# Kernel tuning notes

Hardware: AMD Instinct MI355X
Metric: run time of the kernel (lower is better)

Reference implementation:

```python
import jax, jax.numpy as jnp
import numpy as np

H = 64          # hiddens_dims
K = 3           # Chebyshev order
B = 16          # graphs in batch
NPG = 16384     # nodes per graph
N = B * NPG     # total nodes
E = 2_097_152   # total edges
R = 2191        # num_residues (hard-coded in source)
E_REF = R * 16
HALF = N // 2   # backbone count == sidechain count (mask is balanced per graph)


def _lin(k, fan_in, shape):
    return jax.random.uniform(k, shape, jnp.float32, -1.0, 1.0) / np.sqrt(fan_in)


def setup_inputs() -> dict:
    key = jax.random.key(0)
    ks = jax.random.split(key, 40)
    inp = {}
    inp["x"] = jax.random.normal(ks[0], (N, 3), jnp.float32)
    inp["edge_index"] = jax.random.randint(ks[1], (2, E), 0, N)
    inp["batch"] = jnp.repeat(jnp.arange(B, dtype=jnp.int32), NPG)
    blk = jnp.concatenate([jnp.ones((NPG // 2,), bool), jnp.zeros((NPG // 2,), bool)])
    inp["mask"] = jnp.tile(blk, B)  # backbone=True first half of each graph block
    inp["x_ref"] = jax.random.normal(ks[2], (R, 3), jnp.float32)
    inp["edgeref"] = jax.random.randint(ks[3], (2, E_REF), 0, R)
    i = 4
    for name, cin in [("cw0", 3), ("cw1", H), ("cw2", H), ("rw0", 3), ("rw1", H), ("rw2", H)]:
        inp[name] = _lin(ks[i], cin, (K, cin, H)); i += 1
        inp[name.replace("w", "b")] = jnp.zeros((H,), jnp.float32)  # ChebConv bias init = zeros
    for name, cin, cout in [("mlp_w", 2 * H, H), ("mlpP2_w", 2 * H, H),
                            ("rep0_w", H, H), ("rep1_w", H, H), ("rep2_w", H, 3)]:
        inp[name] = _lin(ks[i], cin, (cin, cout)); i += 1
        inp[name.replace("_w", "_b")] = _lin(ks[i], cin, (cout,)); i += 1
    return inp


def cheb_conv(x, edge_index, W, b, n):
    # PyG ChebConv with sym normalization, lambda_max=2: L_hat = -D^-1/2 A D^-1/2 (diag = 0)
    row, col = edge_index[0], edge_index[1]
    deg = jax.ops.segment_sum(jnp.ones_like(x[:, 0])[row] * 0 + 1.0, row, num_segments=n)
    dinv = jnp.where(deg > 0, jax.lax.rsqrt(jnp.maximum(deg, 1e-12)), 0.0)
    w = -(dinv[row] * dinv[col])  # [E]

    def prop(h):  # L_hat @ h via gather + segment_sum
        return jax.ops.segment_sum(w[:, None] * h[col], row, num_segments=n)

    Tx0 = x
    out = Tx0 @ W[0]
    Tx1 = prop(x)
    out = out + Tx1 @ W[1]
    for k in range(2, K):
        Tx2 = 2.0 * prop(Tx1) - Tx0
        out = out + Tx2 @ W[k]
        Tx0, Tx1 = Tx1, Tx2
    return out + b


def _forward(x, edge_index, mask, x_ref, edgeref,
             cw0, cb0, cw1, cb1, cw2, cb2, rw0, rb0, rw1, rb1, rw2, rb2,
             mlp_w, mlp_b, mlpP2_w, mlpP2_b,
             rep0_w, rep0_b, rep1_w, rep1_b, rep2_w, rep2_b):
    # main GNN stack (tanh after all but last; dropout is identity in eval)
    h = jnp.tanh(cheb_conv(x, edge_index, cw0, cb0, N))
    h = jnp.tanh(cheb_conv(h, edge_index, cw1, cb1, N))
    h = cheb_conv(h, edge_index, cw2, cb2, N)

    bb_idx = jnp.nonzero(mask, size=HALF)[0]
    sc_idx = jnp.nonzero(~mask, size=HALF)[0]
    x_bb = h[bb_idx].reshape(B, -1, H).mean(axis=1)[:, None, :]  # [B,1,H]
    x_sc = h[sc_idx].reshape(B, -1, H).mean(axis=1)[:, None, :]  # [B,1,H]

    # reference-graph stack: source bug makes `conv2 != self.convs[-1]` always True,
    # so tanh follows every convRef layer
    r = jnp.tanh(cheb_conv(x_ref, edgeref, rw0, rb0, R))
    r = jnp.tanh(cheb_conv(r, edgeref, rw1, rb1, R))
    r = jnp.tanh(cheb_conv(r, edgeref, rw2, rb2, R))
    r = jnp.broadcast_to(r[None], (B, R, H))

    bb_rep = jnp.broadcast_to(x_bb, (B, R, H))
    phase1 = jnp.concatenate([r, bb_rep], axis=-1) @ mlp_w + mlp_b        # [B,R,H]
    sc_rep = jnp.broadcast_to(x_sc, (B, R, H))
    phase2 = jnp.concatenate([phase1, sc_rep], axis=-1) @ mlpP2_w + mlpP2_b  # [B,R,H]

    res = phase2.reshape(-1, H)
    res = jax.nn.relu(res @ rep0_w + rep0_b)
    res = jax.nn.relu(res @ rep1_w + rep1_b)
    res = jax.nn.relu(res @ rep2_w + rep2_b)  # [B*R, 3]
    return res.reshape(-1, 3), x_bb, x_sc


def reference(x, edge_index, batch, mask, x_ref, edgeref,
              cw0, cb0, cw1, cb1, cw2, cb2, rw0, rb0, rw1, rb1, rw2, rb2,
              mlp_w, mlp_b, mlpP2_w, mlpP2_b,
              rep0_w, rep0_b, rep1_w, rep1_b, rep2_w, rep2_b):
    del batch  # only used for len(batch.unique()) == B, a static constant here
    return _forward(x, edge_index, mask, x_ref, edgeref,
                    cw0, cb0, cw1, cb1, cw2, cb2, rw0, rb0, rw1, rb1, rw2, rb2,
                    mlp_w, mlp_b, mlpP2_w, mlpP2_b,
                    rep0_w, rep0_b, rep1_w, rep1_b, rep2_w, rep2_b)
```

## Files before the change

kernel.cpp:

```cpp
#include <hip/hip_runtime.h>
#include <hip/hip_fp16.h>
#include <math.h>

#define NN 262144
#define NE 2097152
#define RR 2191
#define ER (RR*16)
#define NB 16
#define BRR (NB*RR)
#define OUT_RES (BRR*3)

typedef __attribute__((ext_vector_type(8))) _Float16 half8;
typedef __attribute__((ext_vector_type(4))) float f32x4;

__global__ void k_histprep(const int* __restrict__ eM, int* __restrict__ degM,
                           unsigned char* __restrict__ rankM,
                           const int* __restrict__ eR, int* __restrict__ degR,
                           unsigned char* __restrict__ rankR,
                           const float* __restrict__ cw1, const float* __restrict__ cw2,
                           const float* __restrict__ rw1, const float* __restrict__ rw2,
                           float* __restrict__ weffC2, float* __restrict__ weffR1,
                           float* __restrict__ weffR2, _Float16* __restrict__ wfragC1,
                           const float* __restrict__ x, float4* __restrict__ x4,
                           const float* __restrict__ x_ref, float4* __restrict__ xr4){
  int b = blockIdx.x, t = threadIdx.x;
  if (b < 2048){
    for (int i = b*256 + t; i < NE; i += 2048*256){
      int old = atomicAdd(&degM[eM[i]], 1);
      rankM[i] = (unsigned char)old;
    }
  } else if (b < 2112){
    for (int i = (b-2048)*256 + t; i < ER; i += 64*256){
      int old = atomicAdd(&degR[eR[i]], 1);
      rankR[i] = (unsigned char)old;
    }
  } else if (b < 2160){
    int y = (b - 2112) >> 4;
    int i = ((b - 2112) & 15)*256 + t;
    const float* W = (y == 0) ? cw2 : (y == 1) ? rw1 : rw2;
    float* D       = (y == 0) ? weffC2 : (y == 1) ? weffR1 : weffR2;
    D[i]        = W[i] - W[8192 + i];
    D[4096 + i] = W[4096 + i];
    D[8192 + i] = 2.0f * W[8192 + i];
  } else if (b < 2208){
    int i = (b - 2160)*256 + t;
    int reg = i & 7, lane = (i >> 3) & 63, nt = (i >> 9) & 3, kc = i >> 11;
    int m = kc >> 1;
    int kin = (kc & 1)*32 + ((lane >> 4) & 3)*8 + reg;
    int n = nt*16 + (lane & 15);
    float eff;
    if      (m == 0) eff = cw1[kin*64 + n] - cw1[8192 + kin*64 + n];
    else if (m == 1) eff = cw1[4096 + kin*64 + n];
    else             eff = 2.0f * cw1[8192 + kin*64 + n];
    wfragC1[i] = (_Float16)eff;
  } else if (b < 3232){
    int i = (b - 2208)*256 + t;
    if (i < NN) x4[i] = make_float4(x[i*3], x[i*3+1], x[i*3+2], 0.0f);
  } else {
    int i = (b - 3232)*256 + t;
    if (i < RR) xr4[i] = make_float4(x_ref[i*3], x_ref[i*3+1], x_ref[i*3+2], 0.0f);
  }
}

__global__ void k_scan1(const int* __restrict__ deg, int* __restrict__ rowptr,
                        int* __restrict__ partials, float* __restrict__ dinv){
  __shared__ int s[256];
  int t = threadIdx.x; int i = blockIdx.x*256 + t;
  int v = deg[i]; s[t] = v; __syncthreads();
  dinv[i] = v > 0 ? 1.0f/sqrtf((float)v) : 0.0f;
  for (int off = 1; off < 256; off <<= 1){
    int x = (t >= off) ? s[t-off] : 0; __syncthreads();
    s[t] += x; __syncthreads();
  }
  rowptr[i] = s[t] - v;
  if (t == 255) partials[blockIdx.x] = s[255];
}

__global__ void __launch_bounds__(1024) k_scan2m(int* __restrict__ partials,
                                                 const int* __restrict__ degR,
                                                 int* __restrict__ rowptrR,
                                                 float* __restrict__ dinvR){
  __shared__ int s[1024];
  int t = threadIdx.x;
  if (blockIdx.x == 0){
    int v = partials[t]; s[t] = v; __syncthreads();
    for (int off = 1; off < 1024; off <<= 1){
      int x = (t >= off) ? s[t-off] : 0; __syncthreads();
      s[t] += x; __syncthreads();
    }
    partials[t] = s[t] - v;
  } else {
    int carry = 0;
    for (int base = 0; base < RR; base += 1024){
      int idx = base + t;
      int v = (idx < RR) ? degR[idx] : 0;
      if (idx < RR) dinvR[idx] = v > 0 ? 1.0f/sqrtf((float)v) : 0.0f;
      s[t] = v; __syncthreads();
      for (int off = 1; off < 1024; off <<= 1){
        int x = (t >= off) ? s[t-off] : 0; __syncthreads();
        s[t] += x; __syncthreads();
      }
      if (idx < RR) rowptrR[idx] = carry + s[t] - v;
      carry += s[1023];
      __syncthreads();
    }
    if (t == 0) rowptrR[RR] = carry;
  }
}

__global__ void k_scan3(int* __restrict__ rowptr, const int* __restrict__ partials){
  int t = threadIdx.x; int i = blockIdx.x*256 + t;
  rowptr[i] += partials[blockIdx.x];
  if (i == 0) rowptr[NN] = NE;
}

__global__ void k_scatter2(const int* __restrict__ eM, const float* __restrict__ dinv,
                           const int* __restrict__ rowptr, const unsigned char* __restrict__ rankM,
                           int2* __restrict__ pair,
                           const int* __restrict__ eR, const float* __restrict__ dinvR,
                           const int* __restrict__ rowptrR, const unsigned char* __restrict__ rankR,
                           int2* __restrict__ pairR){
  int b = blockIdx.x;
  if (b < 2048){
    for (int i = b*256 + threadIdx.x; i < NE; i += 2048*256){
      int r = eM[i], c = eM[NE + i];
      int pos = rowptr[r] + rankM[i];
      unsigned wbits = (unsigned)__float_as_int(-dinv[r]*dinv[c]);
      long long v = (unsigned)c | ((long long)wbits << 32);
      __builtin_nontemporal_store(v, (long long*)(pair + pos));
    }
  } else {
    for (int i = (b-2048)*256 + threadIdx.x; i < ER; i += 64*256){
      int r = eR[i], c = eR[ER + i];
      int pos = rowptrR[r] + rankR[i];
      unsigned wbits = (unsigned)__float_as_int(-dinvR[r]*dinvR[c]);
      long long v = (unsigned)c | ((long long)wbits << 32);
      __builtin_nontemporal_store(v, (long long*)(pairR + pos));
    }
  }
}

__device__ __forceinline__ void prop3_body(const float4* __restrict__ h, float4* __restrict__ y,
                                           const int* __restrict__ rowptr,
                                           const int2* __restrict__ pair, int i){
  float a0 = 0.f, a1 = 0.f, a2 = 0.f;
  int s = rowptr[i], e = rowptr[i+1];
  int p = s;
  for (; p + 4 <= e; p += 4){
    int2 q0 = pair[p], q1 = pair[p+1], q2 = pair[p+2], q3 = pair[p+3];
    float4 v0 = h[q0.x], v1 = h[q1.x], v2 = h[q2.x], v3 = h[q3.x];
    float w0 = __int_as_float(q0.y), w1 = __int_as_float(q1.y);
    float w2 = __int_as_float(q2.y), w3 = __int_as_float(q3.y);
    a0 = fmaf(w0,v0.x, fmaf(w1,v1.x, fmaf(w2,v2.x, fmaf(w3,v3.x, a0))));
    a1 = fmaf(w0,v0.y, fmaf(w1,v1.y, fmaf(w2,v2.y, fmaf(w3,v3.y, a1))));
    a2 = fmaf(w0,v0.z, fmaf(w1,v1.z, fmaf(w2,v2.z, fmaf(w3,v3.z, a2))));
  }
  for (; p < e; p++){
    int2 q = pair[p]; float wv = __int_as_float(q.y);
    float4 v = h[q.x];
    a0 = fmaf(wv, v.x, a0); a1 = fmaf(wv, v.y, a1); a2 = fmaf(wv, v.z, a2);
  }
  y[i] = make_float4(a0, a1, a2, 0.0f);
}

__device__ __forceinline__ void combine3_body(const float4* __restrict__ x,
                                              const float4* __restrict__ t1,
                                              const float4* __restrict__ t2,
                                              const float* __restrict__ W,
                                              const float* __restrict__ bias,
                                              int i, int lane, float* accout){
  float4 px = x[i], p1 = t1[i], p2 = t2[i];
  const float* fx = (const float*)&px;
  const float* f1 = (const float*)&p1;
  const float* f2 = (const float*)&p2;
  float acc = bias[lane];
  #pragma unroll
  for (int j = 0; j < 3; j++){
    float x0 = fx[j], x1 = f1[j];
    float x2 = 2.0f*f2[j] - x0;
    acc += x0*W[      j*64 + lane]
         + x1*W[192 + j*64 + lane]
         + x2*W[384 + j*64 + lane];
  }
  *accout = tanhf(acc);
}

__device__ __forceinline__ void prop64f_body(const float* __restrict__ h, float* __restrict__ y,
                                             const int* __restrict__ rowptr,
                                             const int2* __restrict__ pair, int i, int lane){
  float acc = 0.f;
  int s = rowptr[i], e = rowptr[i+1];
  int p = s;
  for (; p + 4 <= e; p += 4){
    int2 q0 = pair[p], q1 = pair[p+1], q2 = pair[p+2], q3 = pair[p+3];
    float v0 = h[(size_t)q0.x*64 + lane], v1 = h[(size_t)q1.x*64 + lane];
    float v2 = h[(size_t)q2.x*64 + lane], v3 = h[(size_t)q3.x*64 + lane];
    acc = fmaf(__int_as_float(q0.y),v0, fmaf(__int_as_float(q1.y),v1,
          fmaf(__int_as_float(q2.y),v2, fmaf(__int_as_float(q3.y),v3, acc))));
  }
  for (; p < e; p++){
    int2 q = pair[p];
    acc = fmaf(__int_as_float(q.y), h[(size_t)q.x*64 + lane], acc);
  }
  y[(size_t)i*64 + lane] = acc;
}

__device__ __forceinline__ void combine64f_body(const float* __restrict__ A,
                                                const float* __restrict__ Bm,
                                                const float* __restrict__ C,
                                                const float* __restrict__ Weff,
                                                const float* __restrict__ bias,
                                                float* __restrict__ out, int n,
                                                int blk, int t){
  int lane = t & 63;
  int wid  = __builtin_amdgcn_readfirstlane(t >> 6);
  int half_ = wid & 1;
  int row  = blk*128 + (wid >> 1)*64 + lane;
  bool active = (row < n);
  float acc[32];
  #pragma unroll
  for (int c = 0; c < 32; c++) acc[c] = bias[half_*32 + c];
  if (active){
    #pragma unroll 1
    for (int m = 0; m < 3; m++){
      const float* src = (m == 0 ? A : (m == 1 ? Bm : C)) + (size_t)row*64;
      const float* Wm  = Weff + m*4096 + half_*32;
      #pragma unroll 1
      for (int k4 = 0; k4 < 16; k4++){
        float4 a4 = *(const float4*)(src + k4*4);
        const float* wk = Wm + k4*256;
        #pragma unroll
        for (int kk = 0; kk < 4; kk++){
          float a = (kk == 0) ? a4.x : (kk == 1) ? a4.y : (kk == 2) ? a4.z : a4.w;
          #pragma unroll
          for (int c = 0; c < 32; c++)
            acc[c] = fmaf(a, wk[kk*64 + c], acc[c]);
        }
      }
    }
  }
  __syncthreads();
  if (active){
    float* o = out + (size_t)row*64 + half_*32;
    #pragma unroll
    for (int c = 0; c < 32; c++) o[c] = tanhf(acc[c]);
  }
}

__global__ void k_prop3m(const float4* __restrict__ hM, float4* __restrict__ yM,
                         const int* __restrict__ rowptr, const int2* __restrict__ pair,
                         const float4* __restrict__ hR, float4* __restrict__ yR,
                         const int* __restrict__ rowptrR, const int2* __restrict__ pairR){
  int b = blockIdx.x, t = threadIdx.x;
  if (b < 1024){
    prop3_body(hM, yM, rowptr, pair, b*256 + t);
  } else {
    int i = (b - 1024)*256 + t;
    if (i < RR) prop3_body(hR, yR, rowptrR, pairR, i);
  }
}

__global__ void k_combine3m(const float4* __restrict__ x, const float4* __restrict__ t1,
                            const float4* __restrict__ t2, const float* __restrict__ cW,
                            const float* __restrict__ cb, __half* __restrict__ outM,
                            const float4* __restrict__ xr, const float4* __restrict__ r1,
                            const float4* __restrict__ r2, const float* __restrict__ rW,
                            const float* __restrict__ rb, float* __restrict__ outR){
  int b = blockIdx.x, t = threadIdx.x, lane = t & 63;
  if (b < 65536){
    int i = b*4 + (t >> 6);
    float v; combine3_body(x, t1, t2, cW, cb, i, lane, &v);
    outM[(size_t)i*64 + lane] = __float2half_rn(v);
  } else {
    int i = (b - 65536)*4 + (t >> 6);
    if (i < RR){
      float v; combine3_body(xr, r1, r2, rW, rb, i, lane, &v);
      outR[(size_t)i*64 + lane] = v;
    }
  }
}

__global__ void __launch_bounds__(256) k_prop64m(
    const uint4* __restrict__ h4, uint4* __restrict__ y4,
    const int* __restrict__ rowptr, const int2* __restrict__ pair,
    const float* __restrict__ hR, float* __restrict__ yR,
    const int* __restrict__ rowptrR, const int2* __restrict__ pairR){
  int b = blockIdx.x, t = threadIdx.x;
  if (b >= 8192){
    int i = (b - 8192)*4 + (t >> 6);
    if (i < RR) prop64f_body(hR, yR, rowptrR, pairR, i, t & 63);
    return;
  }
  int sub = t & 7;
  int row = b*32 + (t >> 3);
  int s = rowptr[row], e = rowptr[row+1];
  float ac[8];
  #pragma unroll
  for (int k = 0; k < 8; k++) ac[k] = 0.f;
  int p = s;
  for (; p + 8 <= e; p += 8){
    int2 q[8]; uint4 v[8];
    #pragma unroll
    for (int j = 0; j < 8; j++) q[j] = pair[p+j];
    #pragma unroll
    for (int j = 0; j < 8; j++) v[j] = h4[(size_t)q[j].x*8 + sub];
    #pragma unroll
    for (int j = 0; j < 8; j++){
      float wv = __int_as_float(q[j].y);
      #pragma unroll
      for (int k = 0; k < 4; k++){
        float2 f = __half22float2(((const __half2*)&v[j])[k]);
        ac[2*k]   = fmaf(wv, f.x, ac[2*k]);
        ac[2*k+1] = fmaf(wv, f.y, ac[2*k+1]);
      }
    }
  }
  for (; p + 4 <= e; p += 4){
    int2 q[4]; uint4 v[4];
    #pragma unroll
    for (int j = 0; j < 4; j++) q[j] = pair[p+j];
    #pragma unroll
    for (int j = 0; j < 4; j++) v[j] = h4[(size_t)q[j].x*8 + sub];
    #pragma unroll
    for (int j = 0; j < 4; j++){
      float wv = __int_as_float(q[j].y);
      #pragma unroll
      for (int k = 0; k < 4; k++){
        float2 f = __half22float2(((const __half2*)&v[j])[k]);
        ac[2*k]   = fmaf(wv, f.x, ac[2*k]);
        ac[2*k+1] = fmaf(wv, f.y, ac[2*k+1]);
      }
    }
  }
  for (; p < e; p++){
    int2 q = pair[p];
    float wv = __int_as_float(q.y);
    uint4 v = h4[(size_t)q.x*8 + sub];
    #pragma unroll
    for (int k = 0; k < 4; k++){
      float2 f = __half22float2(((const __half2*)&v)[k]);
      ac[2*k]   = fmaf(wv, f.x, ac[2*k]);
      ac[2*k+1] = fmaf(wv, f.y, ac[2*k+1]);
    }
  }
  uint4 r;
  #pragma unroll
  for (int k = 0; k < 4; k++){
    __half2 hp = __floats2half2_rn(ac[2*k], ac[2*k+1]);
    ((unsigned*)&r)[k] = *(unsigned*)&hp;
  }
  y4[(size_t)row*8 + sub] = r;
}

__global__ void __launch_bounds__(256) k_combine64mm(
    const __half* A, const __half* B, const __half* C,
    const _Float16* __restrict__ wfrag, const float* __restrict__ bias,
    __half* out, int ntiles, int wavestride,
    const float* __restrict__ rA, const float* __restrict__ rB, const float* __restrict__ rC,
    const float* __restrict__ weffR, const float* __restrict__ biasR,
    float* __restrict__ outR){
  int t = threadIdx.x;
  if (blockIdx.x >= 1024){
    combine64f_body(rA, rB, rC, weffR, biasR, outR, RR, blockIdx.x - 1024, t);
    return;
  }
  int lane = t & 63;
  int wv = blockIdx.x*4 + (t >> 6);
  half8 bf[24];
  #pragma unroll
  for (int i = 0; i < 24; i++)
    bf[i] = *(const half8*)(wfrag + ((size_t)(i*64 + lane))*8);
  int col = lane & 15, grp = (lane >> 4) & 3;
  float b0 = bias[col], b1 = bias[16+col], b2 = bias[32+col], b3 = bias[48+col];
  for (int tile = wv; tile < ntiles; tile += wavestride){
    size_t rb = (size_t)tile*16;
    f32x4 acc0 = {b0,b0,b0,b0}, acc1 = {b1,b1,b1,b1};
    f32x4 acc2 = {b2,b2,b2,b2}, acc3 = {b3,b3,b3,b3};
    #pragma unroll
    for (int kc = 0; kc < 6; kc++){
      const __half* s = (kc < 2) ? A : (kc < 4) ? B : C;
      half8 a = *(const half8*)(s + (rb + col)*64 + (kc & 1)*32 + grp*8);
      acc0 = __builtin_amdgcn_mfma_f32_16x16x32_f16(a, bf[kc*4+0], acc0, 0,0,0);
      acc1 = __builtin_amdgcn_mfma_f32_16x16x32_f16(a, bf[kc*4+1], acc1, 0,0,0);
      acc2 = __builtin_amdgcn_mfma_f32_16x16x32_f16(a, bf[kc*4+2], acc2, 0,0,0);
      acc3 = __builtin_amdgcn_mfma_f32_16x16x32_f16(a, bf[kc*4+3], acc3, 0,0,0);
    }
    __half* o = out + (rb + grp*4)*64;
    #pragma unroll
    for (int r = 0; r < 4; r++){
      o[(size_t)r*64 +      col] = __float2half_rn(tanhf(acc0[r]));
      o[(size_t)r*64 + 16 + col] = __float2half_rn(tanhf(acc1[r]));
      o[(size_t)r*64 + 32 + col] = __float2half_rn(tanhf(acc2[r]));
      o[(size_t)r*64 + 48 + col] = __float2half_rn(tanhf(acc3[r]));
    }
  }
}

__global__ void k_tail3(const __half2* __restrict__ hA, const __half2* __restrict__ hB,
                        const __half2* __restrict__ hC, float* __restrict__ pA,
                        float* __restrict__ pB, float* __restrict__ pC,
                        const float* __restrict__ rA, const float* __restrict__ rB,
                        const float* __restrict__ rC, const float* __restrict__ weffR,
                        const float* __restrict__ biasR, float* __restrict__ outR){
  int b = blockIdx.x, t = threadIdx.x;
  if (b >= 1536){
    combine64f_body(rA, rB, rC, weffR, biasR, outR, RR, b - 1536, t);
    return;
  }
  int y = b >> 9;
  const __half2* src = (y == 0) ? hA : (y == 1) ? hB : hC;
  float* dst         = (y == 0) ? pA : (y == 1) ? pB : pC;
  int blk = b & 511;
  int chunk = blk & 15, seg = blk >> 4;
  int ch2 = t & 31, rsub = t >> 5;
  int base = seg*8192 + chunk*512;
  float ax = 0.f, ay = 0.f;
  for (int j = 0; j < 64; j++){
    int row = base + rsub + j*8;
    float2 v = __half22float2(src[(size_t)row*32 + ch2]);
    ax += v.x; ay += v.y;
  }
  __shared__ float sx[256], sy[256];
  sx[t] = ax; sy[t] = ay; __syncthreads();
  if (t < 32){
    float tx = 0.f, ty = 0.f;
    #pragma unroll
    for (int j = 0; j < 8; j++){ tx += sx[ch2 + j*32]; ty += sy[ch2 + j*32]; }
    int bb = seg >> 1, half_ = seg & 1;
    atomicAdd(&dst[half_*1024 + bb*64 + ch2*2],     tx);
    atomicAdd(&dst[half_*1024 + bb*64 + ch2*2 + 1], ty);
  }
}

__global__ void k_cpr(const float* __restrict__ pA, const float* __restrict__ pB,
                      const float* __restrict__ pC, const float* __restrict__ weff,
                      const float* __restrict__ bias, float* __restrict__ xbbsc,
                      float* __restrict__ dout,
                      const float* __restrict__ refA, const float* __restrict__ mlp_w,
                      const float* __restrict__ mlp2_w, const float* __restrict__ rep0_w,
                      float* __restrict__ rt3a){
  int b = blockIdx.x, t = threadIdx.x;
  if (b < 8){
    int i = b*256 + t;
    int pr = i >> 6, c = i & 63;
    const float* a = pA + pr*64;
    const float* bb = pB + pr*64;
    const float* cc = pC + pr*64;
    float v = 0.f;
    for (int k = 0; k < 64; k++){
      v = fmaf(a[k],  weff[        k*64 + c], v);
      v = fmaf(bb[k], weff[4096 +  k*64 + c], v);
      v = fmaf(cc[k], weff[8192 +  k*64 + c], v);
    }
    v = v*(1.0f/8192.0f) + bias[c];
    xbbsc[i] = v;
    dout[OUT_RES + i] = v;
  } else {
    int lane = t & 63;
    int i = (b - 8)*4 + (t >> 6);
    if (i >= RR) return;
    float v = refA[i*64 + lane];
    float a = 0.f;
    #pragma unroll
    for (int k = 0; k < 64; k++) a += __shfl(v, k, 64) * mlp_w[k*64 + lane];
    float bb = 0.f;
    #pragma unroll
    for (int k = 0; k < 64; k++) bb += __shfl(a, k, 64) * mlp2_w[k*64 + lane];
    float c = 0.f;
    #pragma unroll
    for (int k = 0; k < 64; k++) c += __shfl(bb, k, 64) * rep0_w[k*64 + lane];
    rt3a[i*64 + lane] = c;
  }
}

__global__ void k_bbchain(const float* __restrict__ xbbsc,
                          const float* __restrict__ mlp_w,  const float* __restrict__ mlp_b,
                          const float* __restrict__ mlp2_w, const float* __restrict__ mlp2_b,
                          const float* __restrict__ rep0_w, const float* __restrict__ rep0_b,
                          float* __restrict__ bt3a){
  int t = threadIdx.x, lane = t & 63;
  int i = blockIdx.x*4 + (t >> 6);
  if (i >= NB) return;
  float vbb = xbbsc[i*64 + lane];
  float vsc = xbbsc[1024 + i*64 + lane];
  float a = mlp_b[lane];
  #pragma unroll
  for (int k = 0; k < 64; k++) a += __shfl(vbb, k, 64) * mlp_w[4096 + k*64 + lane];
  float b = mlp2_b[lane];
  #pragma unroll
  for (int k = 0; k < 64; k++) b += __shfl(a, k, 64) * mlp2_w[k*64 + lane];
  #pragma unroll
  for (int k = 0; k < 64; k++) b += __shfl(vsc, k, 64) * mlp2_w[4096 + k*64 + lane];
  float c = rep0_b[lane];
  #pragma unroll
  for (int k = 0; k < 64; k++) c += __shfl(b, k, 64) * rep0_w[k*64 + lane];
  bt3a[i*64 + lane] = c;
}

__global__ void k_final(const float* __restrict__ rt3, const float* __restrict__ bt3,
                        const float* __restrict__ W1, const float* __restrict__ b1,
                        const float* __restrict__ W2, const float* __restrict__ b2,
                        float* __restrict__ dout){
  int t = threadIdx.x, lane = t & 63;
  int g = blockIdx.x*4 + (t >> 6);
  if (g >= BRR) return;
  int b = g / RR, r = g - b*RR;
  float m = rt3[r*64 + lane] + bt3[b*64 + lane];
  m = fmaxf(m, 0.0f);
  float acc = b1[lane];
  #pragma unroll
  for (int k = 0; k < 64; k++) acc += __shfl(m, k, 64) * W1[k*64 + lane];
  float u = fmaxf(acc, 0.0f);
  float p0 = u*W2[lane*3+0], p1 = u*W2[lane*3+1], p2 = u*W2[lane*3+2];
  #pragma unroll
  for (int off = 32; off > 0; off >>= 1){
    p0 += __shfl_xor(p0, off, 64);
    p1 += __shfl_xor(p1, off, 64);
    p2 += __shfl_xor(p2, off, 64);
  }
  if (lane == 0){
    dout[g*3+0] = fmaxf(p0 + b2[0], 0.0f);
    dout[g*3+1] = fmaxf(p1 + b2[1], 0.0f);
    dout[g*3+2] = fmaxf(p2 + b2[2], 0.0f);
  }
}

extern "C" void kernel_launch(void* const* d_in, const int* in_sizes, int n_in,
                              void* d_out, int out_size, void* d_ws, size_t ws_size,
                              hipStream_t stream){
  const float* x     = (const float*)d_in[0];
  const int*   eidx  = (const int*)d_in[1];
  const float* x_ref = (const float*)d_in[4];
  const int*   eref  = (const int*)d_in[5];
  const float* cw0 = (const float*)d_in[6],  *cb0 = (const float*)d_in[7];
  const float* cw1 = (const float*)d_in[8],  *cb1 = (const float*)d_in[9];
  const float* cw2 = (const float*)d_in[10], *cb2 = (const float*)d_in[11];
  const float* rw0 = (const float*)d_in[12], *rb0 = (const float*)d_in[13];
  const float* rw1 = (const float*)d_in[14], *rb1 = (const float*)d_in[15];
  const float* rw2 = (const float*)d_in[16], *rb2 = (const float*)d_in[17];
  const float* mlp_w  = (const float*)d_in[18], *mlp_b  = (const float*)d_in[19];
  const float* mlp2_w = (const float*)d_in[20], *mlp2_b = (const float*)d_in[21];
  const float* rep0_w = (const float*)d_in[22], *rep0_b = (const float*)d_in[23];
  const float* rep1_w = (const float*)d_in[24], *rep1_b = (const float*)d_in[25];
  const float* rep2_w = (const float*)d_in[26], *rep2_b = (const float*)d_in[27];
  float* out = (float*)d_out;

  char* w = (char*)d_ws;
  size_t off = 0;
  auto alloc = [&](size_t bytes)->void*{
    void* p = w + off;
    off = (off + bytes + 255) & ~(size_t)255;
    return p;
  };
  int*   deg     = (int*)  alloc(NN*4);
  int*   degR    = (int*)  alloc(RR*4);
  float* poolA   = (float*)alloc(2048*4);
  float* poolB   = (float*)alloc(2048*4);
  float* poolC   = (float*)alloc(2048*4);
  size_t zero_bytes = off;

  int*   rowptr   = (int*)  alloc((NN+1)*4);
  int*   partials = (int*)  alloc(1024*4);
  int*   rowptrR  = (int*)  alloc((RR+1)*4);
  float* dinv     = (float*)alloc(NN*4);
  float* dinvR    = (float*)alloc(RR*4);
  unsigned char* rankM = (unsigned char*)alloc(NE);
  unsigned char* rankR = (unsigned char*)alloc(ER);
  int2*  cpair    = (int2*) alloc((size_t)NE*8);
  int2*  cpairR   = (int2*) alloc((size_t)ER*8);
  float4* x4      = (float4*)alloc((size_t)NN*16);
  float4* t1_4    = (float4*)alloc((size_t)NN*16);
  float4* t2_4    = (float4*)alloc((size_t)NN*16);
  float4* xr4     = (float4*)alloc((size_t)RR*16);
  float4* rt1_4   = (float4*)alloc((size_t)RR*16);
  float4* rt2_4   = (float4*)alloc((size_t)RR*16);
  __half* hA      = (__half*)alloc((size_t)NN*64*2);
  __half* hB      = (__half*)alloc((size_t)NN*64*2);
  __half* hC      = (__half*)alloc((size_t)NN*64*2);
  float* refA     = (float*)alloc(RR*64*4);
  float* refB     = (float*)alloc(RR*64*4);
  float* refC     = (float*)alloc(RR*64*4);
  float* xbbsc    = (float*)alloc(2048*4);
  float* rt3a     = (float*)alloc(RR*64*4);
  float* bt3a     = (float*)alloc(NB*64*4);
  float* weffC2   = (float*)alloc(12288*4);
  float* weffR1   = (float*)alloc(12288*4);
  float* weffR2   = (float*)alloc(12288*4);
  _Float16* wfragC1 = (_Float16*)alloc(12288*2);
  (void)ws_size; (void)in_sizes; (void)n_in; (void)out_size;

  hipMemsetAsync(d_ws, 0, zero_bytes, stream);

  k_histprep<<<3241, 256, 0, stream>>>(eidx, deg, rankM, eref, degR, rankR,
                                       cw1, cw2, rw1, rw2,
                                       weffC2, weffR1, weffR2, wfragC1,
                                       x, x4, x_ref, xr4);
  k_scan1<<<1024, 256, 0, stream>>>(deg, rowptr, partials, dinv);
  k_scan2m<<<2, 1024, 0, stream>>>(partials, degR, rowptrR, dinvR);
  k_scan3<<<1024, 256, 0, stream>>>(rowptr, partials);
  k_scatter2<<<2112, 256, 0, stream>>>(eidx, dinv, rowptr, rankM, cpair,
                                       eref, dinvR, rowptrR, rankR, cpairR);

  k_prop3m<<<1033, 256, 0, stream>>>(x4, t1_4, rowptr, cpair, xr4, rt1_4, rowptrR, cpairR);
  k_prop3m<<<1033, 256, 0, stream>>>(t1_4, t2_4, rowptr, cpair, rt1_4, rt2_4, rowptrR, cpairR);
  k_combine3m<<<66084, 256, 0, stream>>>(x4, t1_4, t2_4, cw0, cb0, hA,
                                         xr4, rt1_4, rt2_4, rw0, rb0, refA);
  k_prop64m<<<8740, 256, 0, stream>>>((const uint4*)hA, (uint4*)hB, rowptr, cpair,
                                      refA, refB, rowptrR, cpairR);
  k_prop64m<<<8740, 256, 0, stream>>>((const uint4*)hB, (uint4*)hC, rowptr, cpair,
                                      refB, refC, rowptrR, cpairR);
  k_combine64mm<<<1042, 256, 0, stream>>>(hA, hB, hC, wfragC1, cb1, hA, NN/16, 4096,
                                          refA, refB, refC, weffR1, rb1, refA);
  k_prop64m<<<8740, 256, 0, stream>>>((const uint4*)hA, (uint4*)hB, rowptr, cpair,
                                      refA, refB, rowptrR, cpairR);
  k_prop64m<<<8740, 256, 0, stream>>>((const uint4*)hB, (uint4*)hC, rowptr, cpair,
                                      refB, refC, rowptrR, cpairR);
  k_tail3<<<1554, 256, 0, stream>>>((const __half2*)hA, (const __half2*)hB, (const __half2*)hC,
                                    poolA, poolB, poolC,
                                    refA, refB, refC, weffR2, rb2, refA);
  k_cpr<<<556, 256, 0, stream>>>(poolA, poolB, poolC, weffC2, cb2, xbbsc, out,
                                 refA, mlp_w, mlp2_w, rep0_w, rt3a);
  k_bbchain<<<4, 256, 0, stream>>>(xbbsc, mlp_w, mlp_b, mlp2_w, mlp2_b, rep0_w, rep0_b, bt3a);
  k_final<<<(BRR+3)/4, 256, 0, stream>>>(rt3a, bt3a, rep1_w, rep1_b, rep2_w, rep2_b, out);
}
```

Before: 673.1 us.

## Replace final Chebyshev propagation with pooled column-weight sums and nontemporal edge loads

The last graph propagation (hC = L·hB) is only ever consumed through per-graph, per-half pooling, so it is replaced algebraically. A per-source sigma table (sum of edge weights into each of 32 graph-half segments) is accumulated with atomics inside the first propagation launch, and pooled L·hB is then computed as sigma-weighted sums of hB. This removes one full 64-wide gather-propagation pass. The CSR pair loads become nontemporal, and the small tail kernels are merged into fewer launches. The cost is a 32 MB sigma buffer that must be zeroed each call, plus 2M float atomics, and more work in the reduction blocks.

```diff
diff --git a/kernel.cpp b/kernel.cpp
--- a/kernel.cpp
+++ b/kernel.cpp
@@ -12,6 +12,12 @@
 
 typedef __attribute__((ext_vector_type(8))) _Float16 half8;
 typedef __attribute__((ext_vector_type(4))) float f32x4;
+
+__device__ __forceinline__ int2 ntp(const int2* p){
+  long long v = __builtin_nontemporal_load((const long long*)p);
+  int2 r; r.x = (int)(unsigned)(v & 0xffffffffll); r.y = (int)(unsigned)((unsigned long long)v >> 32);
+  return r;
+}
 
 __global__ void k_histprep(const int* __restrict__ eM, int* __restrict__ degM,
                            unsigned char* __restrict__ rankM,
@@ -147,7 +153,7 @@
   int s = rowptr[i], e = rowptr[i+1];
   int p = s;
   for (; p + 4 <= e; p += 4){
-    int2 q0 = pair[p], q1 = pair[p+1], q2 = pair[p+2], q3 = pair[p+3];
+    int2 q0 = ntp(pair+p), q1 = ntp(pair+p+1), q2 = ntp(pair+p+2), q3 = ntp(pair+p+3);
     float4 v0 = h[q0.x], v1 = h[q1.x], v2 = h[q2.x], v3 = h[q3.x];
     float w0 = __int_as_float(q0.y), w1 = __int_as_float(q1.y);
     float w2 = __int_as_float(q2.y), w3 = __int_as_float(q3.y);
@@ -284,8 +290,18 @@
     const uint4* __restrict__ h4, uint4* __restrict__ y4,
     const int* __restrict__ rowptr, const int2* __restrict__ pair,
     const float* __restrict__ hR, float* __restrict__ yR,
-    const int* __restrict__ rowptrR, const int2* __restrict__ pairR){
+    const int* __restrict__ rowptrR, const int2* __restrict__ pairR,
+    const int* __restrict__ eidx, const float* __restrict__ dinv,
+    float* __restrict__ sigma){
   int b = blockIdx.x, t = threadIdx.x;
+  if (b >= 8740){
+    int sb = b - 8740;
+    for (int i = sb*256 + t; i < NE; i += 512*256){
+      int r = eidx[i], c = eidx[NE + i];
+      atomicAdd(&sigma[(size_t)c*32 + (r >> 13)], -dinv[r]*dinv[c]);
+    }
+    return;
+  }
   if (b >= 8192){
     int i = (b - 8192)*4 + (t >> 6);
     if (i < RR) prop64f_body(hR, yR, rowptrR, pairR, i, t & 63);
@@ -301,7 +317,7 @@
   for (; p + 8 <= e; p += 8){
     int2 q[8]; uint4 v[8];
     #pragma unroll
-    for (int j = 0; j < 8; j++) q[j] = pair[p+j];
+    for (int j = 0; j < 8; j++) q[j] = ntp(pair + p + j);
     #pragma unroll
     for (int j = 0; j < 8; j++) v[j] = h4[(size_t)q[j].x*8 + sub];
     #pragma unroll
@@ -318,7 +334,7 @@
   for (; p + 4 <= e; p += 4){
     int2 q[4]; uint4 v[4];
     #pragma unroll
-    for (int j = 0; j < 4; j++) q[j] = pair[p+j];
+    for (int j = 0; j < 4; j++) q[j] = ntp(pair + p + j);
     #pragma unroll
     for (int j = 0; j < 4; j++) v[j] = h4[(size_t)q[j].x*8 + sub];
     #pragma unroll
@@ -396,49 +412,86 @@
   }
 }
 
-__global__ void k_tail3(const __half2* __restrict__ hA, const __half2* __restrict__ hB,
-                        const __half2* __restrict__ hC, float* __restrict__ pA,
-                        float* __restrict__ pB, float* __restrict__ pC,
-                        const float* __restrict__ rA, const float* __restrict__ rB,
-                        const float* __restrict__ rC, const float* __restrict__ weffR,
-                        const float* __restrict__ biasR, float* __restrict__ outR){
+__global__ void __launch_bounds__(256) k_sigred(
+    const __half2* __restrict__ hA2, const __half2* __restrict__ hB2,
+    const __half* __restrict__ hBh, const float* __restrict__ sigma,
+    float* __restrict__ pA, float* __restrict__ pB, float* __restrict__ pC,
+    const float* __restrict__ rB, float* __restrict__ rC,
+    const int* __restrict__ rowptrR, const int2* __restrict__ pairR){
   int b = blockIdx.x, t = threadIdx.x;
-  if (b >= 1536){
-    combine64f_body(rA, rB, rC, weffR, biasR, outR, RR, b - 1536, t);
-    return;
-  }
-  int y = b >> 9;
-  const __half2* src = (y == 0) ? hA : (y == 1) ? hB : hC;
-  float* dst         = (y == 0) ? pA : (y == 1) ? pB : pC;
-  int blk = b & 511;
-  int chunk = blk & 15, seg = blk >> 4;
-  int ch2 = t & 31, rsub = t >> 5;
-  int base = seg*8192 + chunk*512;
-  float ax = 0.f, ay = 0.f;
-  for (int j = 0; j < 64; j++){
-    int row = base + rsub + j*8;
-    float2 v = __half22float2(src[(size_t)row*32 + ch2]);
-    ax += v.x; ay += v.y;
-  }
-  __shared__ float sx[256], sy[256];
-  sx[t] = ax; sy[t] = ay; __syncthreads();
-  if (t < 32){
-    float tx = 0.f, ty = 0.f;
-    #pragma unroll
-    for (int j = 0; j < 8; j++){ tx += sx[ch2 + j*32]; ty += sy[ch2 + j*32]; }
-    int bb = seg >> 1, half_ = seg & 1;
-    atomicAdd(&dst[half_*1024 + bb*64 + ch2*2],     tx);
-    atomicAdd(&dst[half_*1024 + bb*64 + ch2*2 + 1], ty);
-  }
-}
-
-__global__ void k_cpr(const float* __restrict__ pA, const float* __restrict__ pB,
-                      const float* __restrict__ pC, const float* __restrict__ weff,
-                      const float* __restrict__ bias, float* __restrict__ xbbsc,
-                      float* __restrict__ dout,
-                      const float* __restrict__ refA, const float* __restrict__ mlp_w,
-                      const float* __restrict__ mlp2_w, const float* __restrict__ rep0_w,
-                      float* __restrict__ rt3a){
+  if (b < 1024){
+    const __half2* src = (b < 512) ? hA2 : hB2;
+    float* dst = (b < 512) ? pA : pB;
+    int blk = b & 511;
+    int chunk = blk & 15, seg = blk >> 4;
+    int ch2 = t & 31, rsub = t >> 5;
+    int base = seg*8192 + chunk*512;
+    float ax = 0.f, ay = 0.f;
+    for (int j = 0; j < 64; j++){
+      int row = base + rsub + j*8;
+      float2 v = __half22float2(src[(size_t)row*32 + ch2]);
+      ax += v.x; ay += v.y;
+    }
+    __shared__ float sx[256], sy[256];
+    sx[t] = ax; sy[t] = ay; __syncthreads();
+    if (t < 32){
+      float tx = 0.f, ty = 0.f;
+      #pragma unroll
+      for (int j = 0; j < 8; j++){ tx += sx[ch2 + j*32]; ty += sy[ch2 + j*32]; }
+      int bb = seg >> 1, half_ = seg & 1;
+      atomicAdd(&dst[half_*1024 + bb*64 + ch2*2],     tx);
+      atomicAdd(&dst[half_*1024 + bb*64 + ch2*2 + 1], ty);
+    }
+  } else if (b < 1152){
+    int blk = b - 1024;
+    int ch = t & 63, jsub = t >> 6;
+    float acc[32];
+    #pragma unroll
+    for (int s = 0; s < 32; s++) acc[s] = 0.f;
+    int jend = blk*2048 + 2048;
+    for (int j = blk*2048 + jsub; j < jend; j += 4){
+      float bv = __half2float(hBh[(size_t)j*64 + ch]);
+      const float4* sg = (const float4*)(sigma + (size_t)j*32);
+      #pragma unroll
+      for (int sq = 0; sq < 8; sq++){
+        float4 s4 = sg[sq];
+        acc[sq*4+0] = fmaf(s4.x, bv, acc[sq*4+0]);
+        acc[sq*4+1] = fmaf(s4.y, bv, acc[sq*4+1]);
+        acc[sq*4+2] = fmaf(s4.z, bv, acc[sq*4+2]);
+        acc[sq*4+3] = fmaf(s4.w, bv, acc[sq*4+3]);
+      }
+    }
+    __shared__ float red[32][64];
+    if (jsub == 0){
+      #pragma unroll
+      for (int s = 0; s < 32; s++) red[s][ch] = acc[s];
+    }
+    __syncthreads();
+    #pragma unroll
+    for (int w = 1; w < 4; w++){
+      if (jsub == w){
+        #pragma unroll
+        for (int s = 0; s < 32; s++) red[s][ch] += acc[s];
+      }
+      __syncthreads();
+    }
+    for (int e = t; e < 2048; e += 256){
+      int s = e >> 6, c = e & 63;
+      atomicAdd(&pC[(s & 1)*1024 + (s >> 1)*64 + c], red[s][c]);
+    }
+  } else {
+    int i = (b - 1152)*4 + (t >> 6);
+    if (i < RR) prop64f_body(rB, rC, rowptrR, pairR, i, t & 63);
+  }
+}
+
+__global__ void k_cpr3(const float* __restrict__ pA, const float* __restrict__ pB,
+                       const float* __restrict__ pC, const float* __restrict__ weff,
+                       const float* __restrict__ bias, float* __restrict__ xbbsc,
+                       float* __restrict__ dout,
+                       const float* __restrict__ rA, const float* __restrict__ rB,
+                       const float* __restrict__ rC, const float* __restrict__ weffR,
+                       const float* __restrict__ biasR, float* __restrict__ outR){
   int b = blockIdx.x, t = threadIdx.x;
   if (b < 8){
     int i = b*256 + t;
@@ -456,8 +509,19 @@
     xbbsc[i] = v;
     dout[OUT_RES + i] = v;
   } else {
-    int lane = t & 63;
-    int i = (b - 8)*4 + (t >> 6);
+    combine64f_body(rA, rB, rC, weffR, biasR, outR, RR, b - 8, t);
+  }
+}
+
+__global__ void k_chains(const float* __restrict__ refA, const float* __restrict__ mlp_w,
+                         const float* __restrict__ mlp2_w, const float* __restrict__ rep0_w,
+                         float* __restrict__ rt3a,
+                         const float* __restrict__ xbbsc, const float* __restrict__ mlp_b,
+                         const float* __restrict__ mlp2_b, const float* __restrict__ rep0_b,
+                         float* __restrict__ bt3a){
+  int b = blockIdx.x, t = threadIdx.x, lane = t & 63;
+  if (b < 548){
+    int i = b*4 + (t >> 6);
     if (i >= RR) return;
     float v = refA[i*64 + lane];
     float a = 0.f;
@@ -470,31 +534,24 @@
     #pragma unroll
     for (int k = 0; k < 64; k++) c += __shfl(bb, k, 64) * rep0_w[k*64 + lane];
     rt3a[i*64 + lane] = c;
-  }
-}
-
-__global__ void k_bbchain(const float* __restrict__ xbbsc,
-                          const float* __restrict__ mlp_w,  const float* __restrict__ mlp_b,
-                          const float* __restrict__ mlp2_w, const float* __restrict__ mlp2_b,
-                          const float* __restrict__ rep0_w, const float* __restrict__ rep0_b,
-                          float* __restrict__ bt3a){
-  int t = threadIdx.x, lane = t & 63;
-  int i = blockIdx.x*4 + (t >> 6);
-  if (i >= NB) return;
-  float vbb = xbbsc[i*64 + lane];
-  float vsc = xbbsc[1024 + i*64 + lane];
-  float a = mlp_b[lane];
-  #pragma unroll
-  for (int k = 0; k < 64; k++) a += __shfl(vbb, k, 64) * mlp_w[4096 + k*64 + lane];
-  float b = mlp2_b[lane];
-  #pragma unroll
-  for (int k = 0; k < 64; k++) b += __shfl(a, k, 64) * mlp2_w[k*64 + lane];
-  #pragma unroll
-  for (int k = 0; k < 64; k++) b += __shfl(vsc, k, 64) * mlp2_w[4096 + k*64 + lane];
-  float c = rep0_b[lane];
-  #pragma unroll
-  for (int k = 0; k < 64; k++) c += __shfl(b, k, 64) * rep0_w[k*64 + lane];
-  bt3a[i*64 + lane] = c;
+  } else {
+    int i = (b - 548)*4 + (t >> 6);
+    if (i >= NB) return;
+    float vbb = xbbsc[i*64 + lane];
+    float vsc = xbbsc[1024 + i*64 + lane];
+    float a = mlp_b[lane];
+    #pragma unroll
+    for (int k = 0; k < 64; k++) a += __shfl(vbb, k, 64) * mlp_w[4096 + k*64 + lane];
+    float bb = mlp2_b[lane];
+    #pragma unroll
+    for (int k = 0; k < 64; k++) bb += __shfl(a, k, 64) * mlp2_w[k*64 + lane];
+    #pragma unroll
+    for (int k = 0; k < 64; k++) bb += __shfl(vsc, k, 64) * mlp2_w[4096 + k*64 + lane];
+    float c = rep0_b[lane];
+    #pragma unroll
+    for (int k = 0; k < 64; k++) c += __shfl(bb, k, 64) * rep0_w[k*64 + lane];
+    bt3a[i*64 + lane] = c;
+  }
 }
 
 __global__ void k_final(const float* __restrict__ rt3, const float* __restrict__ bt3,
@@ -557,6 +614,7 @@
   float* poolA   = (float*)alloc(2048*4);
   float* poolB   = (float*)alloc(2048*4);
   float* poolC   = (float*)alloc(2048*4);
+  float* sigma   = (float*)alloc((size_t)NN*32*4);
   size_t zero_bytes = off;
 
   int*   rowptr   = (int*)  alloc((NN+1)*4);
@@ -605,21 +663,20 @@
   k_prop3m<<<1033, 256, 0, stream>>>(t1_4, t2_4, rowptr, cpair, rt1_4, rt2_4, rowptrR, cpairR);
   k_combine3m<<<66084, 256, 0, stream>>>(x4, t1_4, t2_4, cw0, cb0, hA,
                                          xr4, rt1_4, rt2_4, rw0, rb0, refA);
-  k_prop64m<<<8740, 256, 0, stream>>>((const uint4*)hA, (uint4*)hB, rowptr, cpair,
-                                      refA, refB, rowptrR, cpairR);
+  k_prop64m<<<9252, 256, 0, stream>>>((const uint4*)hA, (uint4*)hB, rowptr, cpair,
+                                      refA, refB, rowptrR, cpairR, eidx, dinv, sigma);
   k_prop64m<<<8740, 256, 0, stream>>>((const uint4*)hB, (uint4*)hC, rowptr, cpair,
-                                      refB, refC, rowptrR, cpairR);
+                                      refB, refC, rowptrR, cpairR, eidx, dinv, sigma);
   k_combine64mm<<<1042, 256, 0, stream>>>(hA, hB, hC, wfragC1, cb1, hA, NN/16, 4096,
                                           refA, refB, refC, weffR1, rb1, refA);
   k_prop64m<<<8740, 256, 0, stream>>>((const uint4*)hA, (uint4*)hB, rowptr, cpair,
-                                      refA, refB, rowptrR, cpairR);
-  k_prop64m<<<8740, 256, 0, stream>>>((const uint4*)hB, (uint4*)hC, rowptr, cpair,
-                                      refB, refC, rowptrR, cpairR);
-  k_tail3<<<1554, 256, 0, stream>>>((const __half2*)hA, (const __half2*)hB, (const __half2*)hC,
-                                    poolA, poolB, poolC,
-                                    refA, refB, refC, weffR2, rb2, refA);
-  k_cpr<<<556, 256, 0, stream>>>(poolA, poolB, poolC, weffC2, cb2, xbbsc, out,
-                                 refA, mlp_w, mlp2_w, rep0_w, rt3a);
-  k_bbchain<<<4, 256, 0, stream>>>(xbbsc, mlp_w, mlp_b, mlp2_w, mlp2_b, rep0_w, rep0_b, bt3a);
+                                      refA, refB, rowptrR, cpairR, eidx, dinv, sigma);
+  k_sigred<<<1700, 256, 0, stream>>>((const __half2*)hA, (const __half2*)hB,
+                                     hB, sigma, poolA, poolB, poolC,
+                                     refB, refC, rowptrR, cpairR);
+  k_cpr3<<<26, 256, 0, stream>>>(poolA, poolB, poolC, weffC2, cb2, xbbsc, out,
+                                 refA, refB, refC, weffR2, rb2, refA);
+  k_chains<<<552, 256, 0, stream>>>(refA, mlp_w, mlp2_w, rep0_w, rt3a,
+                                    xbbsc, mlp_b, mlp2_b, rep0_b, bt3a);
   k_final<<<(BRR+3)/4, 256, 0, stream>>>(rt3a, bt3a, rep1_w, rep1_b, rep2_w, rep2_b, out);
 }
```

Result: slower. 966.7 us (+43.6%).

## Fuse mean-pooling of hA/hB into prop kernels and use nontemporal edge loads

Applied to the files above, without the earlier changes.

The pooling of the hA and hB feature buffers moves out of the tail kernel and into the last two propagation launches as extra blocks, so each buffer is reduced while it is already being read nearby. The tail kernel then only pools hC and runs the reference-graph combine. Separately, the CSR edge-pair loads in the propagation kernels become nontemporal loads, aiming to keep the gathered node features resident in cache. The extra pool blocks sit on the tail of the prop grids and may contend for bandwidth with the gather work.

```diff
diff --git a/kernel.cpp b/kernel.cpp
--- a/kernel.cpp
+++ b/kernel.cpp
@@ -12,6 +12,12 @@
 
 typedef __attribute__((ext_vector_type(8))) _Float16 half8;
 typedef __attribute__((ext_vector_type(4))) float f32x4;
+
+__device__ __forceinline__ int2 ntp(const int2* p){
+  long long v = __builtin_nontemporal_load((const long long*)p);
+  int2 r; r.x = (int)(unsigned)(v & 0xffffffffll); r.y = (int)(unsigned)((unsigned long long)v >> 32);
+  return r;
+}
 
 __global__ void k_histprep(const int* __restrict__ eM, int* __restrict__ degM,
                            unsigned char* __restrict__ rankM,
@@ -147,7 +153,7 @@
   int s = rowptr[i], e = rowptr[i+1];
   int p = s;
   for (; p + 4 <= e; p += 4){
-    int2 q0 = pair[p], q1 = pair[p+1], q2 = pair[p+2], q3 = pair[p+3];
+    int2 q0 = ntp(pair+p), q1 = ntp(pair+p+1), q2 = ntp(pair+p+2), q3 = ntp(pair+p+3);
     float4 v0 = h[q0.x], v1 = h[q1.x], v2 = h[q2.x], v3 = h[q3.x];
     float w0 = __int_as_float(q0.y), w1 = __int_as_float(q1.y);
     float w2 = __int_as_float(q2.y), w3 = __int_as_float(q3.y);
@@ -247,6 +253,29 @@
   }
 }
 
+__device__ __forceinline__ void pool_body(const __half2* __restrict__ src,
+                                          float* __restrict__ dst, int blk, int t){
+  int chunk = blk & 15, seg = blk >> 4;
+  int ch2 = t & 31, rsub = t >> 5;
+  int base = seg*8192 + chunk*512;
+  float ax = 0.f, ay = 0.f;
+  for (int j = 0; j < 64; j++){
+    int row = base + rsub + j*8;
+    float2 v = __half22float2(src[(size_t)row*32 + ch2]);
+    ax += v.x; ay += v.y;
+  }
+  __shared__ float sx[256], sy[256];
+  sx[t] = ax; sy[t] = ay; __syncthreads();
+  if (t < 32){
+    float tx = 0.f, ty = 0.f;
+    #pragma unroll
+    for (int j = 0; j < 8; j++){ tx += sx[ch2 + j*32]; ty += sy[ch2 + j*32]; }
+    int bb = seg >> 1, half_ = seg & 1;
+    atomicAdd(&dst[half_*1024 + bb*64 + ch2*2],     tx);
+    atomicAdd(&dst[half_*1024 + bb*64 + ch2*2 + 1], ty);
+  }
+}
+
 __global__ void k_prop3m(const float4* __restrict__ hM, float4* __restrict__ yM,
                          const int* __restrict__ rowptr, const int2* __restrict__ pair,
                          const float4* __restrict__ hR, float4* __restrict__ yR,
@@ -284,8 +313,13 @@
     const uint4* __restrict__ h4, uint4* __restrict__ y4,
     const int* __restrict__ rowptr, const int2* __restrict__ pair,
     const float* __restrict__ hR, float* __restrict__ yR,
-    const int* __restrict__ rowptrR, const int2* __restrict__ pairR){
+    const int* __restrict__ rowptrR, const int2* __restrict__ pairR,
+    const __half2* __restrict__ poolsrc, float* __restrict__ pooldst){
   int b = blockIdx.x, t = threadIdx.x;
+  if (b >= 8740){
+    pool_body(poolsrc, pooldst, b - 8740, t);
+    return;
+  }
   if (b >= 8192){
     int i = (b - 8192)*4 + (t >> 6);
     if (i < RR) prop64f_body(hR, yR, rowptrR, pairR, i, t & 63);
@@ -301,7 +335,7 @@
   for (; p + 8 <= e; p += 8){
     int2 q[8]; uint4 v[8];
     #pragma unroll
-    for (int j = 0; j < 8; j++) q[j] = pair[p+j];
+    for (int j = 0; j < 8; j++) q[j] = ntp(pair + p + j);
     #pragma unroll
     for (int j = 0; j < 8; j++) v[j] = h4[(size_t)q[j].x*8 + sub];
     #pragma unroll
@@ -318,7 +352,7 @@
   for (; p + 4 <= e; p += 4){
     int2 q[4]; uint4 v[4];
     #pragma unroll
-    for (int j = 0; j < 4; j++) q[j] = pair[p+j];
+    for (int j = 0; j < 4; j++) q[j] = ntp(pair + p + j);
     #pragma unroll
     for (int j = 0; j < 4; j++) v[j] = h4[(size_t)q[j].x*8 + sub];
     #pragma unroll
@@ -396,39 +430,15 @@
   }
 }
 
-__global__ void k_tail3(const __half2* __restrict__ hA, const __half2* __restrict__ hB,
-                        const __half2* __restrict__ hC, float* __restrict__ pA,
-                        float* __restrict__ pB, float* __restrict__ pC,
+__global__ void k_tail3(const __half2* __restrict__ hC2, float* __restrict__ pC,
                         const float* __restrict__ rA, const float* __restrict__ rB,
                         const float* __restrict__ rC, const float* __restrict__ weffR,
                         const float* __restrict__ biasR, float* __restrict__ outR){
   int b = blockIdx.x, t = threadIdx.x;
-  if (b >= 1536){
-    combine64f_body(rA, rB, rC, weffR, biasR, outR, RR, b - 1536, t);
-    return;
-  }
-  int y = b >> 9;
-  const __half2* src = (y == 0) ? hA : (y == 1) ? hB : hC;
-  float* dst         = (y == 0) ? pA : (y == 1) ? pB : pC;
-  int blk = b & 511;
-  int chunk = blk & 15, seg = blk >> 4;
-  int ch2 = t & 31, rsub = t >> 5;
-  int base = seg*8192 + chunk*512;
-  float ax = 0.f, ay = 0.f;
-  for (int j = 0; j < 64; j++){
-    int row = base + rsub + j*8;
-    float2 v = __half22float2(src[(size_t)row*32 + ch2]);
-    ax += v.x; ay += v.y;
-  }
-  __shared__ float sx[256], sy[256];
-  sx[t] = ax; sy[t] = ay; __syncthreads();
-  if (t < 32){
-    float tx = 0.f, ty = 0.f;
-    #pragma unroll
-    for (int j = 0; j < 8; j++){ tx += sx[ch2 + j*32]; ty += sy[ch2 + j*32]; }
-    int bb = seg >> 1, half_ = seg & 1;
-    atomicAdd(&dst[half_*1024 + bb*64 + ch2*2],     tx);
-    atomicAdd(&dst[half_*1024 + bb*64 + ch2*2 + 1], ty);
+  if (b < 512){
+    pool_body(hC2, pC, b, t);
+  } else {
+    combine64f_body(rA, rB, rC, weffR, biasR, outR, RR, b - 512, t);
   }
 }
 
@@ -606,18 +616,19 @@
   k_combine3m<<<66084, 256, 0, stream>>>(x4, t1_4, t2_4, cw0, cb0, hA,
                                          xr4, rt1_4, rt2_4, rw0, rb0, refA);
   k_prop64m<<<8740, 256, 0, stream>>>((const uint4*)hA, (uint4*)hB, rowptr, cpair,
-                                      refA, refB, rowptrR, cpairR);
+                                      refA, refB, rowptrR, cpairR, nullptr, nullptr);
   k_prop64m<<<8740, 256, 0, stream>>>((const uint4*)hB, (uint4*)hC, rowptr, cpair,
-                                      refB, refC, rowptrR, cpairR);
+                                      refB, refC, rowptrR, cpairR, nullptr, nullptr);
   k_combine64mm<<<1042, 256, 0, stream>>>(hA, hB, hC, wfragC1, cb1, hA, NN/16, 4096,
                                           refA, refB, refC, weffR1, rb1, refA);
-  k_prop64m<<<8740, 256, 0, stream>>>((const uint4*)hA, (uint4*)hB, rowptr, cpair,
-                                      refA, refB, rowptrR, cpairR);
-  k_prop64m<<<8740, 256, 0, stream>>>((const uint4*)hB, (uint4*)hC, rowptr, cpair,
-                                      refB, refC, rowptrR, cpairR);
-  k_tail3<<<1554, 256, 0, stream>>>((const __half2*)hA, (const __half2*)hB, (const __half2*)hC,
-                                    poolA, poolB, poolC,
-                                    refA, refB, refC, weffR2, rb2, refA);
+  k_prop64m<<<9252, 256, 0, stream>>>((const uint4*)hA, (uint4*)hB, rowptr, cpair,
+                                      refA, refB, rowptrR, cpairR,
+                                      (const __half2*)hA, poolA);
+  k_prop64m<<<9252, 256, 0, stream>>>((const uint4*)hB, (uint4*)hC, rowptr, cpair,
+                                      refB, refC, rowptrR, cpairR,
+                                      (const __half2*)hB, poolB);
+  k_tail3<<<530, 256, 0, stream>>>((const __half2*)hC, poolC,
+                                   refA, refB, refC, weffR2, rb2, refA);
   k_cpr<<<556, 256, 0, stream>>>(poolA, poolB, poolC, weffC2, cb2, xbbsc, out,
                                  refA, mlp_w, mlp2_w, rep0_w, rt3a);
   k_bbchain<<<4, 256, 0, stream>>>(xbbsc, mlp_w, mlp_b, mlp2_w, mlp2_b, rep0_w, rep0_b, bt3a);
```

Result: slower. 687.7 us (+2.2%).
